# Kernel tuning notes

Measured on AMD Instinct MI355X. Metric: run time of the kernel, lower is better.

The kernel has to match this reference:

```python
import jax, jax.numpy as jnp
import numpy as np

HID = 1024
HEADS = 16
DH = HID // HEADS
SCALE = DH ** -0.5
L, B = 2048, 2


def setup_inputs() -> dict:
    key = jax.random.key(0)
    ks = jax.random.split(key, 16)
    inp = {
        "query": jax.random.normal(ks[0], (L, B, HID), jnp.float32),
        "key": jax.random.normal(ks[1], (L, B, HID), jnp.float32),
        "value": jax.random.normal(ks[2], (L, B, HID), jnp.float32),
        "mask": jax.random.randint(ks[3], (B, L), 0, 2).astype(bool),
    }
    # xavier-uniform linear weights (torch Linear stores [out, in]; y = x @ W.T + b)
    lim = (6.0 / (HID + HID)) ** 0.5
    for i, name in enumerate(["wq", "wk", "wv", "wfc"]):
        inp[name] = jax.random.uniform(ks[4 + i], (HID, HID), jnp.float32, -lim, lim)
    inp["bq"] = jnp.zeros((HID,), jnp.float32)
    inp["bk"] = jnp.zeros((HID,), jnp.float32)
    inp["bv"] = jnp.zeros((HID,), jnp.float32)
    inp["bfc"] = jnp.zeros((HID,), jnp.float32)
    inp["tao"] = jnp.full((HEADS,), 10.0, jnp.float32)
    return inp


def reference(query, key, value, mask, wq, bq, wk, bk, wv, bv, wfc, bfc, tao):
    # inputs arrive [L, B, D]; module transposes to [B, L, D]
    q = jnp.swapaxes(query, 0, 1)
    k = jnp.swapaxes(key, 0, 1)
    v = jnp.swapaxes(value, 0, 1)
    bsz, length, _ = q.shape

    def heads(x, w, b):
        y = x @ w.T + b                      # [B, L, D]
        return y.reshape(bsz, length, HEADS, DH).transpose(0, 2, 1, 3)  # [B, H, L, d]

    Q = heads(q, wq, bq)
    K = heads(k, wk, bk)
    V = heads(v, wv, bv)

    qk = jnp.einsum("bhqd,bhkd->bhqk", Q, K) * SCALE  # [B, H, L, L]

    # gaussian positional bias: -|i-j|^2/2 * tao_h^-4
    idx = jnp.arange(length, dtype=jnp.float32)
    dist = -0.5 * (idx[:, None] - idx[None, :]) ** 2          # [L, L]
    qk = qk + dist[None, None, :, :] * (tao ** -4)[None, :, None, None]

    qk = jnp.where(mask[:, None, None, :], -jnp.inf, qk)
    attn = jax.nn.softmax(qk, axis=-1)  # dropout is identity in eval mode

    x = jnp.einsum("bhqk,bhkd->bhqd", attn, V)            # [B, H, L, d]
    x = x.transpose(0, 2, 1, 3).reshape(bsz, length, HID)  # [B, L, D]
    x = x @ wfc.T + bfc
    return jnp.swapaxes(x, 0, 1)  # [L, B, D]
```

## Files before the change

kernel.cpp:

```cpp
#include <hip/hip_runtime.h>

#define LQ   2048
#define BQ   2
#define HID  1024
#define NH   16
#define DH   64
#define SCALE 0.125f
#define L2E  1.44269504088896f
#define C1   0.18033688011f
#define EXPOFF 23.0831206542f

using short8  = __attribute__((ext_vector_type(8))) short;
using ushort8 = __attribute__((ext_vector_type(8))) unsigned short;
using f32x4   = __attribute__((ext_vector_type(4))) float;
typedef unsigned short u16;
typedef __attribute__((ext_vector_type(2))) __bf16 bf16x2;

__device__ inline u16 f2bf(float x) {
    unsigned int u = __float_as_uint(x);
    u = (u + 0x7fffu + ((u >> 16) & 1u)) >> 16;
    return (u16)u;
}

#if defined(__has_builtin)
#if __has_builtin(__builtin_amdgcn_cvt_pk_bf16_f32)
#define HAVE_PKBF 1
#endif
#if __has_builtin(__builtin_amdgcn_exp2f)
#define HAVE_EXP2 1
#endif
#endif

__device__ inline unsigned int pkbf(float a, float b) {
#ifdef HAVE_PKBF
    bf16x2 r = __builtin_amdgcn_cvt_pk_bf16_f32(a, b);
    return __builtin_bit_cast(unsigned int, r);
#else
    return (unsigned int)f2bf(a) | ((unsigned int)f2bf(b) << 16);
#endif
}

__device__ inline float fexp2(float x) {
#ifdef HAVE_EXP2
    return __builtin_amdgcn_exp2f(x);
#else
    return exp2f(x);
#endif
}

__device__ inline void gl_lds16(const u16* g, u16* l) {
    __builtin_amdgcn_global_load_lds(
        (const __attribute__((address_space(1))) void*)g,
        (__attribute__((address_space(3))) void*)l, 16, 0, 0);
}

__global__ __launch_bounds__(256) void maskprep(const unsigned char* __restrict__ mraw,
                                                int* __restrict__ mout, int n) {
    __shared__ int cnt;
    int t = threadIdx.x;
    if (t == 0) cnt = 0;
    __syncthreads();
    int local = 0;
    for (int i = t; i < n; i += 256) {
        if ((i & 3) && mraw[i]) local++;
    }
    atomicAdd(&cnt, local);
    __syncthreads();
    bool isInt32 = (cnt == 0);
    const int* mi = (const int*)mraw;
    for (int i = t; i < n; i += 256) {
        mout[i] = isInt32 ? mi[i] : (int)mraw[i];
    }
}

struct CastArgs {
    const float* s[7];
    u16* d[7];
    int n[7];
};

__global__ __launch_bounds__(256) void castall(CastArgs a) {
    const int y = blockIdx.y;
    const float* s = a.s[y];
    u16* d = a.d[y];
    const int n4 = a.n[y] >> 2;
    for (int i = blockIdx.x * 256 + threadIdx.x; i < n4; i += gridDim.x * 256) {
        float4 v = *(const float4*)(s + (size_t)i * 4);
        uint2 p;
        p.x = pkbf(v.x, v.y);
        p.y = pkbf(v.z, v.w);
        *(uint2*)(d + (size_t)i * 4) = p;
    }
}

struct QkvArgs {
    const u16* A[3];
    const u16* W[3];
    const float* bias[3];
    u16* out[3];
};

__global__ __launch_bounds__(256) void gemm_qkv(QkvArgs ga) {
    __shared__ u16 As[128][32];
    __shared__ u16 Bs[128][32];

    const int z = blockIdx.z;
    const u16* A = ga.A[z];
    const u16* W = ga.W[z];
    const float* bias = ga.bias[z];
    u16* outp = ga.out[z];

    const int t = threadIdx.x;
    const int m0 = blockIdx.x * 128;
    const int n0 = blockIdx.y * 128;
    const int lane = t & 63;
    const int lane15 = lane & 15;
    const int quad = lane >> 4;
    const int w = t >> 6;
    const int wm = (w >> 1) * 64;
    const int wn = (w & 1) * 64;

    const int l4 = lane >> 2;
    const int ch = (lane & 3) ^ ((lane >> 3) & 3);
    const u16* aSrc0 = A + (size_t)(m0 + 32 * w + l4) * HID + 8 * ch;
    const u16* aSrc1 = aSrc0 + (size_t)16 * HID;
    const u16* bSrc0 = W + (size_t)(n0 + 32 * w + l4) * HID + 8 * ch;
    const u16* bSrc1 = bSrc0 + (size_t)16 * HID;
    u16* aDst0 = &As[32 * w][0];
    u16* aDst1 = &As[32 * w + 16][0];
    u16* bDst0 = &Bs[32 * w][0];
    u16* bDst1 = &Bs[32 * w + 16][0];

    const int qp = quad ^ ((lane15 >> 1) & 3);

    f32x4 acc[4][4];
#pragma unroll
    for (int i = 0; i < 4; i++)
#pragma unroll
        for (int j = 0; j < 4; j++) acc[i][j] = (f32x4){0,0,0,0};

    for (int k0 = 0; k0 < HID; k0 += 32) {
        __syncthreads();
        gl_lds16(aSrc0 + k0, aDst0);
        gl_lds16(aSrc1 + k0, aDst1);
        gl_lds16(bSrc0 + k0, bDst0);
        gl_lds16(bSrc1 + k0, bDst1);
        __syncthreads();

        short8 af[4], bf[4];
#pragma unroll
        for (int i = 0; i < 4; i++) {
            af[i] = *(const short8*)&As[wm + i * 16 + lane15][qp * 8];
            bf[i] = *(const short8*)&Bs[wn + i * 16 + lane15][qp * 8];
        }
#pragma unroll
        for (int mi = 0; mi < 4; mi++)
#pragma unroll
            for (int ni = 0; ni < 4; ni++)
                acc[mi][ni] = __builtin_amdgcn_mfma_f32_16x16x32_bf16(af[mi], bf[ni], acc[mi][ni], 0, 0, 0);
    }

#pragma unroll
    for (int mi = 0; mi < 4; mi++) {
#pragma unroll
        for (int ni = 0; ni < 4; ni++) {
            const int n = n0 + wn + ni * 16 + lane15;
            const float bv = bias[n];
            const int h = n >> 6, d = n & 63;
#pragma unroll
            for (int r = 0; r < 4; r++) {
                const int m = m0 + wm + mi * 16 + quad * 4 + r;
                const float c = acc[mi][ni][r] + bv;
                const int b = m & 1, l = m >> 1;
                if (z < 2) {
                    outp[(((size_t)(b * NH + h)) * LQ + l) * DH + d] = f2bf(c);
                } else {
                    outp[(((size_t)(b * NH + h)) * DH + d) * LQ + l] = f2bf(c);
                }
            }
        }
    }
}

__global__ __launch_bounds__(256) void gemm_fc(const u16* __restrict__ A,
                                               const u16* __restrict__ W,
                                               const float* __restrict__ bias,
                                               float* __restrict__ outp) {
    __shared__ u16 As[128][32];
    __shared__ u16 Bs[64][32];

    const int t = threadIdx.x;
    const int m0 = blockIdx.x * 128;
    const int n0 = blockIdx.y * 64;
    const int lane = t & 63;
    const int lane15 = lane & 15;
    const int quad = lane >> 4;
    const int w = t >> 6;
    const int wm = (w >> 1) * 64;
    const int wn = (w & 1) * 32;

    const int l4 = lane >> 2;
    const int ch = (lane & 3) ^ ((lane >> 3) & 3);
    const u16* aSrc0 = A + (size_t)(m0 + 32 * w + l4) * HID + 8 * ch;
    const u16* aSrc1 = aSrc0 + (size_t)16 * HID;
    const u16* bSrc0 = W + (size_t)(n0 + 16 * w + l4) * HID + 8 * ch;
    u16* aDst0 = &As[32 * w][0];
    u16* aDst1 = &As[32 * w + 16][0];
    u16* bDst0 = &Bs[16 * w][0];

    const int qp = quad ^ ((lane15 >> 1) & 3);

    f32x4 acc[4][2];
#pragma unroll
    for (int i = 0; i < 4; i++)
#pragma unroll
        for (int j = 0; j < 2; j++) acc[i][j] = (f32x4){0,0,0,0};

    for (int k0 = 0; k0 < HID; k0 += 32) {
        __syncthreads();
        gl_lds16(aSrc0 + k0, aDst0);
        gl_lds16(aSrc1 + k0, aDst1);
        gl_lds16(bSrc0 + k0, bDst0);
        __syncthreads();

        short8 af[4], bf[2];
#pragma unroll
        for (int i = 0; i < 4; i++)
            af[i] = *(const short8*)&As[wm + i * 16 + lane15][qp * 8];
#pragma unroll
        for (int j = 0; j < 2; j++)
            bf[j] = *(const short8*)&Bs[wn + j * 16 + lane15][qp * 8];
#pragma unroll
        for (int mi = 0; mi < 4; mi++)
#pragma unroll
            for (int ni = 0; ni < 2; ni++)
                acc[mi][ni] = __builtin_amdgcn_mfma_f32_16x16x32_bf16(af[mi], bf[ni], acc[mi][ni], 0, 0, 0);
    }

#pragma unroll
    for (int mi = 0; mi < 4; mi++) {
#pragma unroll
        for (int ni = 0; ni < 2; ni++) {
            const int n = n0 + wn + ni * 16 + lane15;
            const float bv = bias[n];
#pragma unroll
            for (int r = 0; r < 4; r++) {
                const int m = m0 + wm + mi * 16 + quad * 4 + r;
                outp[(size_t)m * HID + n] = acc[mi][ni][r] + bv;
            }
        }
    }
}

#define KSTR 72

__global__ __launch_bounds__(512) void attn_kernel(const u16* __restrict__ Qg,
                                                   const u16* __restrict__ Kg,
                                                   const u16* __restrict__ Vtg,
                                                   const int* __restrict__ maskI,
                                                   const float* __restrict__ tao,
                                                   u16* __restrict__ Xa) {
    __shared__ u16 Ks[64][KSTR];
    __shared__ u16 Vt[64][KSTR];
    __shared__ u16 PT[128][KSTR];
    __shared__ float smask[64];

    const int bh = blockIdx.x;
    const int q0 = blockIdx.y * 128;
    const int b = bh >> 4;
    const int h = bh & 15;
    const int t = threadIdx.x;
    const int w = t >> 6;
    const int lane = t & 63;
    const int lane15 = lane & 15;
    const int quad = lane >> 4;

    const u16* Kbase = Kg + (size_t)bh * LQ * DH;
    const u16* Vtbase = Vtg + (size_t)bh * DH * LQ;
    const int* mrow = maskI + b * LQ;

    const float tv = tao[h];
    const float t2 = tv * tv;
    const float nb = -0.5f / (t2 * t2);
    const float nb2 = nb * L2E;
    const float skipd2 = -40.0f / nb2;

    const int qrow = q0 + w * 16 + lane15;
    short8 qB0, qB1;
    {
        const u16* qp = Qg + ((size_t)bh * LQ + qrow) * DH + quad * 8;
        qB0 = *(const short8*)(qp);
        qB1 = *(const short8*)(qp + 32);
    }

    f32x4 O[4];
#pragma unroll
    for (int mt = 0; mt < 4; mt++) O[mt] = (f32x4){0,0,0,0};
    float l_ = 0.0f;

    const float ebase0 = (float)(qrow - quad * 4);
    const int prow = w * 16 + lane15;

    for (int k0 = 0; k0 < LQ; k0 += 64) {
        {
            int dmin = 0;
            if (k0 > q0 + 127) dmin = k0 - (q0 + 127);
            else if (k0 + 63 < q0) dmin = q0 - (k0 + 63);
            const float df = (float)dmin;
            if (df * df > skipd2) continue;
        }
        __syncthreads();
        {
            const int r = t & 63;
            const int c0 = (t >> 6) * 8;
            *(ushort8*)&Ks[r][c0] = *(const ushort8*)(Kbase + (size_t)(k0 + r) * DH + c0);
            *(ushort8*)&Vt[r][c0] = *(const ushort8*)(Vtbase + (size_t)r * LQ + k0 + c0);
            if (t < 64) smask[t] = mrow[k0 + t] ? -3.0e38f : -EXPOFF;
        }
        __syncthreads();

        f32x4 S[4];
#pragma unroll
        for (int kt = 0; kt < 4; kt++) {
            const short8 ka = *(const short8*)&Ks[kt * 16 + lane15][quad * 8];
            const short8 kb = *(const short8*)&Ks[kt * 16 + lane15][32 + quad * 8];
            S[kt] = __builtin_amdgcn_mfma_f32_16x16x32_bf16(ka, qB0, (f32x4){0,0,0,0}, 0, 0, 0);
            S[kt] = __builtin_amdgcn_mfma_f32_16x16x32_bf16(kb, qB1, S[kt], 0, 0, 0);
        }

        const float ebase = ebase0 - (float)k0;
        float lacc = 0.0f;
#pragma unroll
        for (int kt = 0; kt < 4; kt++) {
            const float4 sm4 = *(const float4*)&smask[kt * 16 + quad * 4];
            float p[4];
#pragma unroll
            for (int r = 0; r < 4; r++) {
                const float d = ebase - (float)(kt * 16 + r);
                const float dd = d * d;
                const float tb = fmaf(nb2, dd, ((const float*)&sm4)[r]);
                p[r] = fexp2(fmaf(S[kt][r], C1, tb));
                lacc += p[r];
            }
            uint2 pk2;
            pk2.x = pkbf(p[0], p[1]);
            pk2.y = pkbf(p[2], p[3]);
            *(uint2*)&PT[prow][kt * 16 + quad * 4] = pk2;
        }
        l_ += lacc;

        __syncthreads();

        {
            const short8 pB0 = *(const short8*)&PT[prow][quad * 8];
            const short8 pB1 = *(const short8*)&PT[prow][32 + quad * 8];
#pragma unroll
            for (int mt = 0; mt < 4; mt++) {
                const short8 va = *(const short8*)&Vt[mt * 16 + lane15][quad * 8];
                const short8 vb = *(const short8*)&Vt[mt * 16 + lane15][32 + quad * 8];
                O[mt] = __builtin_amdgcn_mfma_f32_16x16x32_bf16(va, pB0, O[mt], 0, 0, 0);
                O[mt] = __builtin_amdgcn_mfma_f32_16x16x32_bf16(vb, pB1, O[mt], 0, 0, 0);
            }
        }
    }

    l_ += __shfl_xor(l_, 16, 64);
    l_ += __shfl_xor(l_, 32, 64);

    {
        const float inv = 1.0f / l_;
        u16* dst = Xa + ((size_t)qrow * BQ + b) * HID + h * DH;
#pragma unroll
        for (int mt = 0; mt < 4; mt++) {
            uint2 pk2;
            pk2.x = pkbf(O[mt][0] * inv, O[mt][1] * inv);
            pk2.y = pkbf(O[mt][2] * inv, O[mt][3] * inv);
            *(uint2*)(dst + mt * 16 + quad * 4) = pk2;
        }
    }
}

extern "C" void kernel_launch(void* const* d_in, const int* in_sizes, int n_in,
                              void* d_out, int out_size, void* d_ws, size_t ws_size,
                              hipStream_t stream) {
    const float* q    = (const float*)d_in[0];
    const float* k    = (const float*)d_in[1];
    const float* v    = (const float*)d_in[2];
    const void*  mask = d_in[3];
    const float* wq   = (const float*)d_in[4];
    const float* wk   = (const float*)d_in[5];
    const float* wv   = (const float*)d_in[6];
    const float* wfc  = (const float*)d_in[7];
    const float* bq   = (const float*)d_in[8];
    const float* bk   = (const float*)d_in[9];
    const float* bv   = (const float*)d_in[10];
    const float* bfc  = (const float*)d_in[11];
    const float* tao  = (const float*)d_in[12];

    const size_t NE = (size_t)LQ * BQ * HID;
    const size_t NW = (size_t)HID * HID;
    u16* base = (u16*)d_ws;
    u16* Qp    = base;
    u16* Kp    = base + NE;
    u16* Vtp   = base + 2 * NE;
    u16* Xa    = base + 3 * NE;
    u16* qbf   = base + 4 * NE;
    u16* kbf   = base + 5 * NE;
    u16* vbf   = base + 6 * NE;
    u16* wqbf  = base + 7 * NE;
    u16* wkbf  = wqbf + NW;
    u16* wvbf  = wkbf + NW;
    u16* wfcbf = wvbf + NW;
    int* maskI = (int*)(wfcbf + NW);

    maskprep<<<1, 256, 0, stream>>>((const unsigned char*)mask, maskI, BQ * LQ);

    CastArgs ca;
    ca.s[0] = q;   ca.d[0] = qbf;   ca.n[0] = (int)NE;
    ca.s[1] = k;   ca.d[1] = kbf;   ca.n[1] = (int)NE;
    ca.s[2] = v;   ca.d[2] = vbf;   ca.n[2] = (int)NE;
    ca.s[3] = wq;  ca.d[3] = wqbf;  ca.n[3] = (int)NW;
    ca.s[4] = wk;  ca.d[4] = wkbf;  ca.n[4] = (int)NW;
    ca.s[5] = wv;  ca.d[5] = wvbf;  ca.n[5] = (int)NW;
    ca.s[6] = wfc; ca.d[6] = wfcbf; ca.n[6] = (int)NW;
    castall<<<dim3(512, 7), 256, 0, stream>>>(ca);

    QkvArgs ga;
    ga.A[0] = qbf;  ga.W[0] = wqbf;  ga.bias[0] = bq;  ga.out[0] = Qp;
    ga.A[1] = kbf;  ga.W[1] = wkbf;  ga.bias[1] = bk;  ga.out[1] = Kp;
    ga.A[2] = vbf;  ga.W[2] = wvbf;  ga.bias[2] = bv;  ga.out[2] = Vtp;
    gemm_qkv<<<dim3(32, 8, 3), 256, 0, stream>>>(ga);

    attn_kernel<<<dim3(32, 16), 512, 0, stream>>>(Qp, Kp, Vtp, maskI, tao, Xa);

    gemm_fc<<<dim3(32, 16), 256, 0, stream>>>(Xa, wfcbf, bfc, (float*)d_out);
}
```

Measured before the change: 252.7 us.

## Fuse activation cast into QKV GEMM, merge maskprep, widen attention tiles with async LDS loads

The QKV GEMM now loads fp32 activations directly into LDS with swizzled global_load_lds and converts them to bf16 when building fragments, so the separate activation cast and its bf16 round trip through memory go away. The mask preparation is folded into the weight-cast launch as an extra grid row, which removes one kernel launch. The attention kernel processes 128 keys per tile instead of 64, loads K and V with direct-to-LDS loads into XOR-swizzled unpadded layouts, and drops one barrier per half-tile. In exchange the GEMM doubles its A-tile LDS footprint and does the conversion work in each block, and the attention kernel uses more LDS and has coarser distance-based tile skipping.

```diff
diff --git a/kernel.cpp b/kernel.cpp
--- a/kernel.cpp
+++ b/kernel.cpp
@@ -48,43 +48,44 @@
 #endif
 }
 
-__device__ inline void gl_lds16(const u16* g, u16* l) {
+__device__ inline void gl_lds16(const void* g, void* l) {
     __builtin_amdgcn_global_load_lds(
         (const __attribute__((address_space(1))) void*)g,
         (__attribute__((address_space(3))) void*)l, 16, 0, 0);
 }
 
-__global__ __launch_bounds__(256) void maskprep(const unsigned char* __restrict__ mraw,
-                                                int* __restrict__ mout, int n) {
-    __shared__ int cnt;
-    int t = threadIdx.x;
-    if (t == 0) cnt = 0;
-    __syncthreads();
-    int local = 0;
-    for (int i = t; i < n; i += 256) {
-        if ((i & 3) && mraw[i]) local++;
-    }
-    atomicAdd(&cnt, local);
-    __syncthreads();
-    bool isInt32 = (cnt == 0);
-    const int* mi = (const int*)mraw;
-    for (int i = t; i < n; i += 256) {
-        mout[i] = isInt32 ? mi[i] : (int)mraw[i];
-    }
-}
-
 struct CastArgs {
-    const float* s[7];
-    u16* d[7];
-    int n[7];
+    const float* s[4];
+    u16* d[4];
+    int n;
+    const unsigned char* mraw;
+    int* mout;
+    int mn;
 };
 
-__global__ __launch_bounds__(256) void castall(CastArgs a) {
+__global__ __launch_bounds__(256) void castw(CastArgs a) {
     const int y = blockIdx.y;
+    const int t = threadIdx.x;
+    if (y == 4) {
+        if (blockIdx.x != 0) return;
+        __shared__ int cnt;
+        if (t == 0) cnt = 0;
+        __syncthreads();
+        int local = 0;
+        for (int i = t; i < a.mn; i += 256)
+            if ((i & 3) && a.mraw[i]) local++;
+        atomicAdd(&cnt, local);
+        __syncthreads();
+        bool isInt32 = (cnt == 0);
+        const int* mi = (const int*)a.mraw;
+        for (int i = t; i < a.mn; i += 256)
+            a.mout[i] = isInt32 ? mi[i] : (int)a.mraw[i];
+        return;
+    }
     const float* s = a.s[y];
     u16* d = a.d[y];
-    const int n4 = a.n[y] >> 2;
-    for (int i = blockIdx.x * 256 + threadIdx.x; i < n4; i += gridDim.x * 256) {
+    const int n4 = a.n >> 2;
+    for (int i = blockIdx.x * 256 + t; i < n4; i += gridDim.x * 256) {
         float4 v = *(const float4*)(s + (size_t)i * 4);
         uint2 p;
         p.x = pkbf(v.x, v.y);
@@ -94,18 +95,18 @@
 }
 
 struct QkvArgs {
-    const u16* A[3];
+    const float* A[3];
     const u16* W[3];
     const float* bias[3];
     u16* out[3];
 };
 
 __global__ __launch_bounds__(256) void gemm_qkv(QkvArgs ga) {
-    __shared__ u16 As[128][32];
+    __shared__ float Asf[128][32];
     __shared__ u16 Bs[128][32];
 
     const int z = blockIdx.z;
-    const u16* A = ga.A[z];
+    const float* A = ga.A[z];
     const u16* W = ga.W[z];
     const float* bias = ga.bias[z];
     u16* outp = ga.out[z];
@@ -120,17 +121,17 @@
     const int wm = (w >> 1) * 64;
     const int wn = (w & 1) * 64;
 
-    const int l4 = lane >> 2;
-    const int ch = (lane & 3) ^ ((lane >> 3) & 3);
-    const u16* aSrc0 = A + (size_t)(m0 + 32 * w + l4) * HID + 8 * ch;
-    const u16* aSrc1 = aSrc0 + (size_t)16 * HID;
-    const u16* bSrc0 = W + (size_t)(n0 + 32 * w + l4) * HID + 8 * ch;
-    const u16* bSrc1 = bSrc0 + (size_t)16 * HID;
-    u16* aDst0 = &As[32 * w][0];
-    u16* aDst1 = &As[32 * w + 16][0];
-    u16* bDst0 = &Bs[32 * w][0];
-    u16* bDst1 = &Bs[32 * w + 16][0];
-
+    const int arow = 8 * w + (lane >> 3);
+    const int ach = (lane & 7) ^ ((lane >> 3) & 7);
+    const float* aS = A + (size_t)(m0 + arow) * HID + 4 * ach;
+    const int brow = 32 * w + (lane >> 2);
+    const int bch = (lane & 3) ^ ((lane >> 3) & 3);
+    const u16* bS0 = W + (size_t)(n0 + brow) * HID + 8 * bch;
+    const u16* bS1 = bS0 + (size_t)16 * HID;
+    u16* bD0 = &Bs[32 * w][0];
+    u16* bD1 = &Bs[32 * w + 16][0];
+
+    const int sa = lane15 & 7;
     const int qp = quad ^ ((lane15 >> 1) & 3);
 
     f32x4 acc[4][4];
@@ -141,16 +142,23 @@
 
     for (int k0 = 0; k0 < HID; k0 += 32) {
         __syncthreads();
-        gl_lds16(aSrc0 + k0, aDst0);
-        gl_lds16(aSrc1 + k0, aDst1);
-        gl_lds16(bSrc0 + k0, bDst0);
-        gl_lds16(bSrc1 + k0, bDst1);
+#pragma unroll
+        for (int i = 0; i < 4; i++)
+            gl_lds16(aS + (size_t)(32 * i) * HID + k0, &Asf[32 * i + (8 * w)][0]);
+        gl_lds16(bS0 + k0, bD0);
+        gl_lds16(bS1 + k0, bD1);
         __syncthreads();
 
         short8 af[4], bf[4];
 #pragma unroll
         for (int i = 0; i < 4; i++) {
-            af[i] = *(const short8*)&As[wm + i * 16 + lane15][qp * 8];
+            const float* ap = &Asf[wm + i * 16 + lane15][0];
+            const float4 fa = *(const float4*)(ap + 4 * ((2 * quad) ^ sa));
+            const float4 fb = *(const float4*)(ap + 4 * ((2 * quad + 1) ^ sa));
+            uint4 ui;
+            ui.x = pkbf(fa.x, fa.y); ui.y = pkbf(fa.z, fa.w);
+            ui.z = pkbf(fb.x, fb.y); ui.w = pkbf(fb.z, fb.w);
+            af[i] = __builtin_bit_cast(short8, ui);
             bf[i] = *(const short8*)&Bs[wn + i * 16 + lane15][qp * 8];
         }
 #pragma unroll
@@ -252,7 +260,7 @@
     }
 }
 
-#define KSTR 72
+#define PSTR 72
 
 __global__ __launch_bounds__(512) void attn_kernel(const u16* __restrict__ Qg,
                                                    const u16* __restrict__ Kg,
@@ -260,10 +268,10 @@
                                                    const int* __restrict__ maskI,
                                                    const float* __restrict__ tao,
                                                    u16* __restrict__ Xa) {
-    __shared__ u16 Ks[64][KSTR];
-    __shared__ u16 Vt[64][KSTR];
-    __shared__ u16 PT[128][KSTR];
-    __shared__ float smask[64];
+    __shared__ u16 Ks[128][64];
+    __shared__ u16 Vt[64][128];
+    __shared__ u16 PT[128][PSTR];
+    __shared__ float smask[128];
 
     const int bh = blockIdx.x;
     const int q0 = blockIdx.y * 128;
@@ -288,10 +296,24 @@
     const int qrow = q0 + w * 16 + lane15;
     short8 qB0, qB1;
     {
-        const u16* qp = Qg + ((size_t)bh * LQ + qrow) * DH + quad * 8;
-        qB0 = *(const short8*)(qp);
-        qB1 = *(const short8*)(qp + 32);
-    }
+        const u16* qp_ = Qg + ((size_t)bh * LQ + qrow) * DH + quad * 8;
+        qB0 = *(const short8*)(qp_);
+        qB1 = *(const short8*)(qp_ + 32);
+    }
+
+    const int krow = 8 * w + (lane >> 3);
+    const int kch = (lane & 7) ^ ((lane >> 3) & 7);
+    const u16* kS = Kbase + (size_t)krow * DH + 8 * kch;
+    const int vrow = 4 * w + (lane >> 4);
+    const int vch = (lane & 8) | ((lane & 7) ^ (vrow & 7));
+    const u16* vS = Vtbase + (size_t)vrow * LQ + 8 * vch;
+    u16* kD0 = &Ks[8 * w][0];
+    u16* kD1 = &Ks[64 + 8 * w][0];
+    u16* vD0 = &Vt[4 * w][0];
+    u16* vD1 = &Vt[32 + 4 * w][0];
+
+    const int s0 = (quad ^ (lane15 & 7)) * 8;
+    const int s1 = ((4 + quad) ^ (lane15 & 7)) * 8;
 
     f32x4 O[4];
 #pragma unroll
@@ -301,63 +323,62 @@
     const float ebase0 = (float)(qrow - quad * 4);
     const int prow = w * 16 + lane15;
 
-    for (int k0 = 0; k0 < LQ; k0 += 64) {
+    for (int k0 = 0; k0 < LQ; k0 += 128) {
         {
             int dmin = 0;
             if (k0 > q0 + 127) dmin = k0 - (q0 + 127);
-            else if (k0 + 63 < q0) dmin = q0 - (k0 + 63);
+            else if (k0 + 127 < q0) dmin = q0 - (k0 + 127);
             const float df = (float)dmin;
             if (df * df > skipd2) continue;
         }
         __syncthreads();
-        {
-            const int r = t & 63;
-            const int c0 = (t >> 6) * 8;
-            *(ushort8*)&Ks[r][c0] = *(const ushort8*)(Kbase + (size_t)(k0 + r) * DH + c0);
-            *(ushort8*)&Vt[r][c0] = *(const ushort8*)(Vtbase + (size_t)r * LQ + k0 + c0);
-            if (t < 64) smask[t] = mrow[k0 + t] ? -3.0e38f : -EXPOFF;
-        }
-        __syncthreads();
-
-        f32x4 S[4];
-#pragma unroll
-        for (int kt = 0; kt < 4; kt++) {
-            const short8 ka = *(const short8*)&Ks[kt * 16 + lane15][quad * 8];
-            const short8 kb = *(const short8*)&Ks[kt * 16 + lane15][32 + quad * 8];
-            S[kt] = __builtin_amdgcn_mfma_f32_16x16x32_bf16(ka, qB0, (f32x4){0,0,0,0}, 0, 0, 0);
-            S[kt] = __builtin_amdgcn_mfma_f32_16x16x32_bf16(kb, qB1, S[kt], 0, 0, 0);
-        }
-
-        const float ebase = ebase0 - (float)k0;
-        float lacc = 0.0f;
-#pragma unroll
-        for (int kt = 0; kt < 4; kt++) {
-            const float4 sm4 = *(const float4*)&smask[kt * 16 + quad * 4];
-            float p[4];
-#pragma unroll
-            for (int r = 0; r < 4; r++) {
-                const float d = ebase - (float)(kt * 16 + r);
-                const float dd = d * d;
-                const float tb = fmaf(nb2, dd, ((const float*)&sm4)[r]);
-                p[r] = fexp2(fmaf(S[kt][r], C1, tb));
-                lacc += p[r];
+        gl_lds16(kS + (size_t)k0 * DH, kD0);
+        gl_lds16(kS + (size_t)(k0 + 64) * DH, kD1);
+        gl_lds16(vS + k0, vD0);
+        gl_lds16(vS + (size_t)32 * LQ + k0, vD1);
+        if (t < 128) smask[t] = mrow[k0 + t] ? -3.0e38f : -EXPOFF;
+        __syncthreads();
+
+#pragma unroll
+        for (int hh = 0; hh < 2; hh++) {
+            const int kbase = 64 * hh;
+            f32x4 S[4];
+#pragma unroll
+            for (int kt = 0; kt < 4; kt++) {
+                const u16* kr = &Ks[kbase + kt * 16 + lane15][0];
+                const short8 ka = *(const short8*)(kr + s0);
+                const short8 kb = *(const short8*)(kr + s1);
+                S[kt] = __builtin_amdgcn_mfma_f32_16x16x32_bf16(ka, qB0, (f32x4){0,0,0,0}, 0, 0, 0);
+                S[kt] = __builtin_amdgcn_mfma_f32_16x16x32_bf16(kb, qB1, S[kt], 0, 0, 0);
             }
-            uint2 pk2;
-            pk2.x = pkbf(p[0], p[1]);
-            pk2.y = pkbf(p[2], p[3]);
-            *(uint2*)&PT[prow][kt * 16 + quad * 4] = pk2;
-        }
-        l_ += lacc;
-
-        __syncthreads();
-
-        {
+
+            const float ebase = ebase0 - (float)(k0 + kbase);
+            float lacc = 0.0f;
+#pragma unroll
+            for (int kt = 0; kt < 4; kt++) {
+                const float4 sm4 = *(const float4*)&smask[kbase + kt * 16 + quad * 4];
+                float p[4];
+#pragma unroll
+                for (int r = 0; r < 4; r++) {
+                    const float d = ebase - (float)(kt * 16 + r);
+                    const float tb = fmaf(nb2 * d, d, ((const float*)&sm4)[r]);
+                    p[r] = fexp2(fmaf(S[kt][r], C1, tb));
+                    lacc += p[r];
+                }
+                uint2 pk2;
+                pk2.x = pkbf(p[0], p[1]);
+                pk2.y = pkbf(p[2], p[3]);
+                *(uint2*)&PT[prow][kt * 16 + quad * 4] = pk2;
+            }
+            l_ += lacc;
+
             const short8 pB0 = *(const short8*)&PT[prow][quad * 8];
             const short8 pB1 = *(const short8*)&PT[prow][32 + quad * 8];
 #pragma unroll
             for (int mt = 0; mt < 4; mt++) {
-                const short8 va = *(const short8*)&Vt[mt * 16 + lane15][quad * 8];
-                const short8 vb = *(const short8*)&Vt[mt * 16 + lane15][32 + quad * 8];
+                const u16* vr = &Vt[mt * 16 + lane15][kbase];
+                const short8 va = *(const short8*)(vr + s0);
+                const short8 vb = *(const short8*)(vr + s1);
                 O[mt] = __builtin_amdgcn_mfma_f32_16x16x32_bf16(va, pB0, O[mt], 0, 0, 0);
                 O[mt] = __builtin_amdgcn_mfma_f32_16x16x32_bf16(vb, pB1, O[mt], 0, 0, 0);
             }
@@ -404,31 +425,27 @@
     u16* Kp    = base + NE;
     u16* Vtp   = base + 2 * NE;
     u16* Xa    = base + 3 * NE;
-    u16* qbf   = base + 4 * NE;
-    u16* kbf   = base + 5 * NE;
-    u16* vbf   = base + 6 * NE;
-    u16* wqbf  = base + 7 * NE;
+    u16* wqbf  = base + 4 * NE;
     u16* wkbf  = wqbf + NW;
     u16* wvbf  = wkbf + NW;
     u16* wfcbf = wvbf + NW;
     int* maskI = (int*)(wfcbf + NW);
 
-    maskprep<<<1, 256, 0, stream>>>((const unsigned char*)mask, maskI, BQ * LQ);
-
     CastArgs ca;
-    ca.s[0] = q;   ca.d[0] = qbf;   ca.n[0] = (int)NE;
-    ca.s[1] = k;   ca.d[1] = kbf;   ca.n[1] = (int)NE;
-    ca.s[2] = v;   ca.d[2] = vbf;   ca.n[2] = (int)NE;
-    ca.s[3] = wq;  ca.d[3] = wqbf;  ca.n[3] = (int)NW;
-    ca.s[4] = wk;  ca.d[4] = wkbf;  ca.n[4] = (int)NW;
-    ca.s[5] = wv;  ca.d[5] = wvbf;  ca.n[5] = (int)NW;
-    ca.s[6] = wfc; ca.d[6] = wfcbf; ca.n[6] = (int)NW;
-    castall<<<dim3(512, 7), 256, 0, stream>>>(ca);
+    ca.s[0] = wq;  ca.d[0] = wqbf;
+    ca.s[1] = wk;  ca.d[1] = wkbf;
+    ca.s[2] = wv;  ca.d[2] = wvbf;
+    ca.s[3] = wfc; ca.d[3] = wfcbf;
+    ca.n = (int)NW;
+    ca.mraw = (const unsigned char*)mask;
+    ca.mout = maskI;
+    ca.mn = BQ * LQ;
+    castw<<<dim3(256, 5), 256, 0, stream>>>(ca);
 
     QkvArgs ga;
-    ga.A[0] = qbf;  ga.W[0] = wqbf;  ga.bias[0] = bq;  ga.out[0] = Qp;
-    ga.A[1] = kbf;  ga.W[1] = wkbf;  ga.bias[1] = bk;  ga.out[1] = Kp;
-    ga.A[2] = vbf;  ga.W[2] = wvbf;  ga.bias[2] = bv;  ga.out[2] = Vtp;
+    ga.A[0] = q;  ga.W[0] = wqbf;  ga.bias[0] = bq;  ga.out[0] = Qp;
+    ga.A[1] = k;  ga.W[1] = wkbf;  ga.bias[1] = bk;  ga.out[1] = Kp;
+    ga.A[2] = v;  ga.W[2] = wvbf;  ga.bias[2] = bv;  ga.out[2] = Vtp;
     gemm_qkv<<<dim3(32, 8, 3), 256, 0, stream>>>(ga);
 
     attn_kernel<<<dim3(32, 16), 512, 0, stream>>>(Qp, Kp, Vtp, maskI, tao, Xa);
```

Measured after the change: 245.7 us. 2.8% less time.
